# Performance work log

Measured on AMD Instinct MI355X. Metric: run time of the kernel, lower is better.

The kernel has to match this reference:

```python
import jax, jax.numpy as jnp
import numpy as np

T, B, C, N, H = 10, 128, 512, 16, 16
D = C // H          # head dim = 32
HID = 2048          # mlp hidden = 4*dim
TAU, THR, SCALE, ALPHA_MIX = 2.0, 1.0, 0.25, 0.5
SG_ALPHA = 4.0      # surrogate sigmoid alpha

@jax.custom_vjp
def spike_fn(x):
    # heaviside forward, sigmoid surrogate backward (MyGrad / sigmoid.apply)
    return (x > 0).astype(x.dtype)

def _spike_fwd(x):
    return spike_fn(x), x

def _spike_bwd(x, g):
    s = jax.nn.sigmoid(SG_ALPHA * x)
    return (g * SG_ALPHA * s * (1.0 - s),)

spike_fn.defvjp(_spike_fwd, _spike_bwd)

def lif(x):
    # multi-step LIF over leading T axis; mem_detach=True => no BPTT through mem
    def step(mem, inp):
        mem = jax.lax.stop_gradient(mem)
        mem = mem + (inp - mem) / TAU
        s = spike_fn(mem - THR)
        mem = mem * (1.0 - jax.lax.stop_gradient(s))
        return mem, s
    return jax.lax.scan(step, jnp.zeros_like(x[0]), x)[1]

def lif_step(mem, inp):
    # single-step LIF (step=1, layer_by_layer=False); state persists across calls
    mem = jax.lax.stop_gradient(mem)
    mem = mem + (inp - mem) / TAU
    s = spike_fn(mem - THR)
    mem = mem * (1.0 - jax.lax.stop_gradient(s))
    return s, mem

def bn(x, p):
    # eval-mode BatchNorm1d over channel dim; x: (T,B,C,N), p: (4,C)=gamma,beta,mean,var
    g, b, m, v = p
    inv = g * jax.lax.rsqrt(v + 1e-5)
    return (x - m[None, None, :, None]) * inv[None, None, :, None] + b[None, None, :, None]

def conv1x1(x, W):
    # Conv1d k=1 == channel GEMM; x: (T,B,Cin,N), W: (Cout,Cin)
    return jnp.einsum('oc,tbcn->tbon', W, x)

def ssa(x, Wq, bn_q, Wk, bn_k, Wv, bn_v, Wproj, bn_proj, ti_w, ti_b):
    def qkv(W, p):
        y = lif(bn(conv1x1(x, W), p))                       # (T,B,C,N) spikes
        # faithful to torch: raw reshape (T,B,C,N)->(T,B,N,H,D) then permute
        return y.reshape(T, B, N, H, D).transpose(0, 1, 3, 2, 4)  # (T,B,H,N,D)
    q = qkv(Wq, bn_q)
    k = qkv(Wk, bn_k)
    v = qkv(Wv, bn_v)

    out0 = (q[0] @ jnp.swapaxes(k[0], -2, -1) * SCALE) @ v[0]   # (B,H,N,D)

    def step(carry, qkv_t):
        q_ti, mem1, mem2 = carry
        qt, kt, vt = qkv_t
        c = q_ti.reshape(B * H, N, D)
        c = jax.lax.conv_general_dilated(
            c, ti_w, (1,), ((2, 2),), dimension_numbers=('NCH', 'OIH', 'NCH'))
        c = c + ti_b[None, :, None]
        c = c.reshape(B, H, N, D)
        s1, mem1 = lif_step(mem1, c)
        mix = s1 * ALPHA_MIX + qt * (1.0 - ALPHA_MIX)
        s2, mem2 = lif_step(mem2, mix)
        attn = (s2 @ jnp.swapaxes(kt, -2, -1) * SCALE) @ vt
        return (s2, mem1, mem2), attn

    init = (q[0], jnp.zeros_like(q[0]), jnp.zeros_like(q[0]))
    _, outs = jax.lax.scan(step, init, (q[1:], k[1:], v[1:]))
    out = jnp.concatenate([out0[None], outs], axis=0)           # (T,B,H,N,D)

    y = jnp.swapaxes(out, 3, 4).reshape(T, B, C, N)
    y = lif(y)                                                  # attn_lif
    y = lif(bn(conv1x1(y, Wproj), bn_proj))                     # proj
    return y

def mlp(x, W1, b1, bn1, W2, b2, bn2):
    h = lif(bn(conv1x1(x, W1) + b1[None, None, :, None], bn1))
    return lif(bn(conv1x1(h, W2) + b2[None, None, :, None], bn2))

def block(x, Wq, Wk, Wv, Wproj, bn_q, bn_k, bn_v, bn_proj, ti_w, ti_b,
          W1, b1, bn1, W2, b2, bn2):
    x = x + ssa(x, Wq, bn_q, Wk, bn_k, Wv, bn_v, Wproj, bn_proj, ti_w, ti_b)
    x = x + mlp(x, W1, b1, bn1, W2, b2, bn2)
    return x

def setup_inputs() -> dict:
    key = jax.random.key(0)
    ks = jax.random.split(key, 16)

    def w(k, o, i):
        return (jax.random.normal(k, (o, i), jnp.float32) / np.float32(np.sqrt(i)))

    def bnp(k, c):
        k1, k2, k3, k4 = jax.random.split(k, 4)
        return jnp.stack([
            jax.random.uniform(k1, (c,), jnp.float32) + 0.5,   # gamma
            jax.random.normal(k2, (c,), jnp.float32) * 0.1,    # beta
            jax.random.normal(k3, (c,), jnp.float32) * 0.1,    # running mean
            jax.random.uniform(k4, (c,), jnp.float32) + 0.5,   # running var
        ])

    return {
        'x': jax.random.normal(ks[0], (T, B, C, N), jnp.float32),
        'Wq': w(ks[1], C, C), 'Wk': w(ks[2], C, C), 'Wv': w(ks[3], C, C),
        'Wproj': w(ks[4], C, C),
        'bn_q': bnp(ks[5], C), 'bn_k': bnp(ks[6], C), 'bn_v': bnp(ks[7], C),
        'bn_proj': bnp(ks[8], C),
        'ti_w': jax.random.normal(ks[9], (16, 16, 5), jnp.float32) / np.float32(np.sqrt(16 * 5)),
        'ti_b': jax.random.normal(ks[10], (16,), jnp.float32) * 0.1,
        'W1': w(ks[11], HID, C), 'b1': jax.random.normal(ks[12], (HID,), jnp.float32) * 0.1,
        'bn1': bnp(ks[13], HID),
        'W2': w(ks[14], C, HID), 'b2': jax.random.normal(ks[15], (C,), jnp.float32) * 0.1,
        'bn2': bnp(jax.random.fold_in(key, 99), C),
    }

def reference(x, Wq, Wk, Wv, Wproj, bn_q, bn_k, bn_v, bn_proj, ti_w, ti_b,
              W1, b1, bn1, W2, b2, bn2):
    return block(x, Wq, Wk, Wv, Wproj, bn_q, bn_k, bn_v, bn_proj, ti_w, ti_b,
                 W1, b1, bn1, W2, b2, bn2)
```

## Files before the change

kernel.cpp:

```cpp
#include <hip/hip_runtime.h>
#include <cstdint>
#include <cstddef>

#define T_   10
#define B_   128
#define CH_  512
#define N_   16
#define H_   16
#define HID_ 2048
#define TB_  (T_ * B_)

#define BS_PKT   0
#define BS_BF16T 1
#define EP_QKV  0
#define EP_SPK  1
#define EP_HS   2
#define EP_OUT  3

typedef __attribute__((ext_vector_type(8))) short bf16x8;
typedef __attribute__((ext_vector_type(4))) float f32x4;
typedef unsigned short u16;
typedef unsigned long long u64;

__device__ __forceinline__ short f2b(float f) {
    uint32_t u = __float_as_uint(f);
    return (short)((u + 0x7FFFu + ((u >> 16) & 1u)) >> 16);
}
__device__ __forceinline__ float b2f(short s) {
    return __uint_as_float(((uint32_t)(uint16_t)s) << 16);
}

__global__ void fold2(const float* __restrict__ W, const float* __restrict__ bnp,
                      const float* __restrict__ eb, int M, int K, int o0,
                      short* __restrict__ Ah, short* __restrict__ Al,
                      float* __restrict__ bias) {
    int idx = blockIdx.x * 256 + threadIdx.x;
    if (idx >= M * K) return;
    int o = idx / K, k = idx - o * K;
    float g  = bnp[o];
    float be = bnp[M + o];
    float mu = bnp[2 * M + o];
    float va = bnp[3 * M + o];
    float inv = g * (1.0f / sqrtf(va + 1e-5f));
    float w = W[idx] * inv;
    short h = f2b(w);
    Ah[(size_t)(o0 + o) * K + k] = h;
    Al[(size_t)(o0 + o) * K + k] = f2b(w - b2f(h));
    if (k == 0) bias[o0 + o] = ((eb ? eb[o] : 0.0f) - mu) * inv + be;
}

__global__ __launch_bounds__(256) void splitx(
    const float* __restrict__ X, const u16* __restrict__ S,
    short* __restrict__ Bh, short* __restrict__ Bl) {
    __shared__ float xs[8192];
    const int slab = blockIdx.x;
    const int tid  = threadIdx.x;
    const int t    = slab / B_;
    const int b    = slab - t * B_;
    const float* xp = X + (size_t)slab * 8192;
    for (int i = tid; i < 2048; i += 256) {
        float4 v = *(const float4*)&xp[i * 4];
        if (S) {
            union { u16 s[4]; uint2 v; } sw;
            sw.v = *(const uint2*)&S[(size_t)b * 8192 + i * 4];
            v.x += (float)((sw.s[0] >> t) & 1);
            v.y += (float)((sw.s[1] >> t) & 1);
            v.z += (float)((sw.s[2] >> t) & 1);
            v.w += (float)((sw.s[3] >> t) & 1);
        }
        *(float4*)&xs[i * 4] = v;
    }
    __syncthreads();
    const int n = tid & 15, kc = tid >> 4;
    size_t orow = ((size_t)slab * 16 + n) * 512 + kc * 32;
#pragma unroll
    for (int i8 = 0; i8 < 4; ++i8) {
        union { short s[8]; uint4 v; } hb, lb;
#pragma unroll
        for (int j = 0; j < 8; ++j) {
            float v = xs[(kc * 32 + i8 * 8 + j) * 16 + n];
            short h = f2b(v);
            hb.s[j] = h;
            lb.s[j] = f2b(v - b2f(h));
        }
        *(uint4*)&Bh[orow + i8 * 8] = hb.v;
        *(uint4*)&Bl[orow + i8 * 8] = lb.v;
    }
}

template <int R, int GX, int BS, int EPI>
__global__ __launch_bounds__(256, 2) void gemm_mfma(
    const short* __restrict__ Ah, const short* __restrict__ Al,
    const float* __restrict__ bias,
    const short* __restrict__ Bh, const short* __restrict__ Bl,
    const u16* __restrict__ Bu,
    u16* __restrict__ O0, u16* __restrict__ O1, u16* __restrict__ O2,
    float* __restrict__ Oout, const float* __restrict__ Xr,
    const u16* __restrict__ Sr, int K) {
    constexpr int NP = (BS == BS_PKT) ? 2 : 3;
    __shared__ __align__(16) short Bs[(NP == 3 ? 2 : 1) * 6400];
    short* BsH = Bs;
    short* BsL = Bs + 6400;
    const int tid  = threadIdx.x;
    const int lane = tid & 63;
    const int wv   = tid >> 6;
    const int fid  = blockIdx.x;
    const int xcd  = fid & 7;
    const int slot = fid >> 3;
    const int brow = slot / GX;
    const int xb   = slot - brow * GX;
    const int b    = (brow << 3) | xcd;
    const int l15  = lane & 15;
    const int q    = lane >> 4;
    const int row0 = xb * (R * 64) + wv * (R * 16);

    f32x4 acc[R][10];
#pragma unroll
    for (int r = 0; r < R; ++r)
#pragma unroll
        for (int t = 0; t < 10; ++t) acc[r][t] = 0.0f;

    for (int k0 = 0; k0 < K; k0 += 32) {
        __syncthreads();
        if constexpr (BS == BS_PKT) {
            if (tid < 128) {
                int qu = tid & 3, n = (tid >> 2) & 15, half = tid >> 6;
                size_t g = ((size_t)b * 16 + n) * (size_t)K + k0 + qu * 8;
                union { u16 s[8]; uint4 v; } w;
                w.v = *(const uint4*)&Bu[g];
                const int t0 = half * 5;
#pragma unroll
                for (int tt = 0; tt < 5; ++tt) {
                    int t = t0 + tt;
                    union { short s[8]; uint4 v; } hb;
#pragma unroll
                    for (int j = 0; j < 8; ++j)
                        hb.s[j] = ((w.s[j] >> t) & 1) ? (short)0x3F80 : (short)0;
                    *(uint4*)&BsH[(t * 16 + n) * 40 + qu * 8] = hb.v;
                }
            }
        } else {
            for (int idx = tid; idx < 640; idx += 256) {
                int qu = idx & 3, n = (idx >> 2) & 15, t = idx >> 6;
                size_t g = ((size_t)(t * B_ + b) * 16 + n) * (size_t)K + k0 + qu * 8;
                *(uint4*)&BsH[(t * 16 + n) * 40 + qu * 8] = *(const uint4*)&Bh[g];
                *(uint4*)&BsL[(t * 16 + n) * 40 + qu * 8] = *(const uint4*)&Bl[g];
            }
        }
        __syncthreads();
        bf16x8 ah[R], al[R];
#pragma unroll
        for (int r = 0; r < R; ++r) {
            size_t ga = (size_t)(row0 + r * 16 + l15) * K + k0 + q * 8;
            ah[r] = *(const bf16x8*)&Ah[ga];
            al[r] = *(const bf16x8*)&Al[ga];
        }
#pragma unroll
        for (int t = 0; t < 10; ++t) {
            bf16x8 bh = *(const bf16x8*)&BsH[(t * 16 + l15) * 40 + q * 8];
            bf16x8 bl;
            if constexpr (NP == 3) bl = *(const bf16x8*)&BsL[(t * 16 + l15) * 40 + q * 8];
#pragma unroll
            for (int r = 0; r < R; ++r) {
                acc[r][t] = __builtin_amdgcn_mfma_f32_16x16x32_bf16(ah[r], bh, acc[r][t], 0, 0, 0);
                acc[r][t] = __builtin_amdgcn_mfma_f32_16x16x32_bf16(al[r], bh, acc[r][t], 0, 0, 0);
                if constexpr (NP == 3)
                    acc[r][t] = __builtin_amdgcn_mfma_f32_16x16x32_bf16(ah[r], bl, acc[r][t], 0, 0, 0);
            }
        }
    }

    const int tok = l15;
#pragma unroll
    for (int r = 0; r < R; ++r) {
        u16 m4[4];
#pragma unroll
        for (int reg = 0; reg < 4; ++reg) {
            const int row = row0 + r * 16 + q * 4 + reg;
            const float bsv = bias[row];
            u16 sv = 0;
            if constexpr (EPI == EP_OUT) sv = Sr[(size_t)b * 8192 + (size_t)row * 16 + tok];
            float mem = 0.0f;
            u16 msk = 0;
#pragma unroll
            for (int t = 0; t < 10; ++t) {
                float u = acc[r][t][reg] + bsv;
                mem += (u - mem) * 0.5f;
                bool s = mem > 1.0f;
                if (s) mem = 0.0f;
                msk |= (u16)((s ? 1u : 0u) << t);
                if constexpr (EPI == EP_OUT) {
                    size_t off = (size_t)(t * B_ + b) * 8192 + (size_t)row * 16 + tok;
                    Oout[off] = Xr[off] + (float)((sv >> t) & 1) + (s ? 1.0f : 0.0f);
                }
            }
            if constexpr (EPI == EP_QKV) {
                int tsr = row >> 9;
                int c   = row & 511;
                int hh  = (c & 31) >> 1;
                int dd  = ((c & 1) << 4) | tok;
                int nn  = c >> 5;
                u16* qp = (tsr == 0) ? O0 : ((tsr == 1) ? O1 : O2);
                qp[(size_t)b * 8192 + (size_t)hh * 512 + dd * 16 + nn] = msk;
            } else if constexpr (EPI == EP_SPK) {
                O0[(size_t)b * 8192 + (size_t)row * 16 + tok] = msk;
            } else if constexpr (EPI == EP_HS) {
                m4[reg] = msk;
            }
        }
        if constexpr (EPI == EP_HS) {
            union { u16 s[4]; uint2 v; } pk;
            pk.s[0] = m4[0]; pk.s[1] = m4[1]; pk.s[2] = m4[2]; pk.s[3] = m4[3];
            *(uint2*)&O0[((size_t)b * 16 + tok) * 2048 + row0 + r * 16 + q * 4] = pk.v;
        }
    }
}

__global__ __launch_bounds__(256, 1) void scan_kernel(
    const u16* __restrict__ qs, const u16* __restrict__ ks,
    const u16* __restrict__ vs, const float* __restrict__ tiw,
    const float* __restrict__ tib, u16* __restrict__ y1pk) {
    __shared__ float qS[4][36 * 20];
    __shared__ float kS[4][32 * 20];
    __shared__ float vS[4][32 * 20];
    __shared__ float qbS[4][32 * 20];
    __shared__ float A[4][16 * 17];
    const int l  = threadIdx.x & 63;
    const int w  = threadIdx.x >> 6;
    const int b  = blockIdx.y;
    const int h  = blockIdx.x * 4 + w;
    const int n  = l & 15, dg = l >> 4;
    float* qSw  = qS[w];
    float* kSw  = kS[w];
    float* vSw  = vS[w];
    float* qbSw = qbS[w];
    float* Aw   = A[w];

    float wreg[80];
#pragma unroll
    for (int j = 0; j < 80; ++j) wreg[j] = tiw[n * 80 + j];
    const float tibr = tib[n];

    if (l < 40) { qSw[l] = 0.0f; qSw[680 + l] = 0.0f; }

    const size_t base = (size_t)b * 8192 + (size_t)h * 512 + (size_t)l * 8;
    union { u16 s[8]; uint4 v; } qw, kw, vw;
    qw.v = *(const uint4*)&qs[base];
    kw.v = *(const uint4*)&ks[base];
    vw.v = *(const uint4*)&vs[base];

#pragma unroll
    for (int j = 0; j < 8; ++j) {
        int f = l * 8 + j, d = f >> 4, m = f & 15;
        qSw[(d + 2) * 20 + m] = (float)(qw.s[j] & 1);
        kSw[d * 20 + m]       = (float)(kw.s[j] & 1);
        vSw[d * 20 + m]       = (float)(vw.s[j] & 1);
    }

    float mem1[8] = {}, mem2[8] = {}, mem3[8] = {};
    u16 ym[8] = {};

    auto attn_step = [&](int t) {
        float dots[4] = {0.0f, 0.0f, 0.0f, 0.0f};
#pragma unroll
        for (int d = 0; d < 32; ++d) {
            float qv = qSw[(d + 2) * 20 + n];
#pragma unroll
            for (int jj = 0; jj < 4; ++jj)
                dots[jj] = fmaf(qv, kSw[d * 20 + dg * 4 + jj], dots[jj]);
        }
#pragma unroll
        for (int jj = 0; jj < 4; ++jj) Aw[n * 17 + dg * 4 + jj] = dots[jj] * 0.25f;
        float o[8] = {};
#pragma unroll
        for (int m = 0; m < 16; ++m) {
            float av = Aw[n * 17 + m];
#pragma unroll
            for (int dd = 0; dd < 8; ++dd)
                o[dd] = fmaf(av, vSw[(dg * 8 + dd) * 20 + m], o[dd]);
        }
#pragma unroll
        for (int dd = 0; dd < 8; ++dd) {
            mem3[dd] += (o[dd] - mem3[dd]) * 0.5f;
            bool s3 = mem3[dd] > 1.0f;
            if (s3) mem3[dd] = 0.0f;
            ym[dd] |= (u16)((s3 ? 1u : 0u) << t);
        }
    };

    attn_step(0);

    for (int t = 1; t < T_; ++t) {
#pragma unroll
        for (int j = 0; j < 8; ++j) {
            int f = l * 8 + j, d = f >> 4, m = f & 15;
            qbSw[d * 20 + m] = (float)((qw.s[j] >> t) & 1);
            kSw[d * 20 + m]  = (float)((kw.s[j] >> t) & 1);
            vSw[d * 20 + m]  = (float)((vw.s[j] >> t) & 1);
        }
        float c[8];
#pragma unroll
        for (int dd = 0; dd < 8; ++dd) c[dd] = tibr;
#pragma unroll
        for (int x = 0; x < 12; ++x) {
            const float* rp = &qSw[(dg * 8 + x) * 20];
            float qrow[16];
            *(float4*)&qrow[0]  = *(const float4*)&rp[0];
            *(float4*)&qrow[4]  = *(const float4*)&rp[4];
            *(float4*)&qrow[8]  = *(const float4*)&rp[8];
            *(float4*)&qrow[12] = *(const float4*)&rp[12];
#pragma unroll
            for (int k = 0; k < 5; ++k) {
                const int o = x - k;
                if (o >= 0 && o < 8) {
#pragma unroll
                    for (int i = 0; i < 16; ++i)
                        c[o] = fmaf(wreg[i * 5 + k], qrow[i], c[o]);
                }
            }
        }
#pragma unroll
        for (int dd = 0; dd < 8; ++dd) {
            mem1[dd] += (c[dd] - mem1[dd]) * 0.5f;
            bool s1 = mem1[dd] > 1.0f;
            if (s1) mem1[dd] = 0.0f;
            float qb = qbSw[(dg * 8 + dd) * 20 + n];
            float mix = 0.5f * (s1 ? 1.0f : 0.0f) + 0.5f * qb;
            mem2[dd] += (mix - mem2[dd]) * 0.5f;
            bool s2 = mem2[dd] > 1.0f;
            if (s2) mem2[dd] = 0.0f;
            qSw[(dg * 8 + dd + 2) * 20 + n] = s2 ? 1.0f : 0.0f;
        }
        attn_step(t);
    }

    union { u16 s[8]; uint4 v; } yv;
#pragma unroll
    for (int dd = 0; dd < 8; ++dd) yv.s[dd] = ym[dd];
    *(uint4*)&y1pk[((size_t)b * 16 + n) * 512 + h * 32 + dg * 8] = yv.v;
}

extern "C" void kernel_launch(void* const* d_in, const int* in_sizes, int n_in,
                              void* d_out, int out_size, void* d_ws, size_t ws_size,
                              hipStream_t stream) {
    const float* x    = (const float*)d_in[0];
    const float* Wq   = (const float*)d_in[1];
    const float* Wk   = (const float*)d_in[2];
    const float* Wv   = (const float*)d_in[3];
    const float* Wp   = (const float*)d_in[4];
    const float* bnq  = (const float*)d_in[5];
    const float* bnk  = (const float*)d_in[6];
    const float* bnv  = (const float*)d_in[7];
    const float* bnpj = (const float*)d_in[8];
    const float* tiw  = (const float*)d_in[9];
    const float* tib  = (const float*)d_in[10];
    const float* W1   = (const float*)d_in[11];
    const float* b1   = (const float*)d_in[12];
    const float* bn1  = (const float*)d_in[13];
    const float* W2   = (const float*)d_in[14];
    const float* b2   = (const float*)d_in[15];
    const float* bn2  = (const float*)d_in[16];
    float* out = (float*)d_out;

    char* ws = (char*)d_ws;
    size_t cur = 0;
    auto alloc = [&](size_t bytes) -> void* {
        void* p = ws + cur;
        cur = (cur + bytes + 255) & ~(size_t)255;
        return p;
    };
    const size_t PKQ = (size_t)B_ * 8192;
    u16* qpk  = (u16*)alloc(4 * PKQ * 2);
    u16* kpk  = qpk + PKQ;
    u16* vpk  = qpk + 2 * PKQ;
    u16* y1pk = qpk + 3 * PKQ;
    u16* hspk = qpk;
    u16* spk  = (u16*)alloc(PKQ * 2);
    short* BhT = (short*)alloc((size_t)TB_ * 16 * 512 * 2);
    short* BlT = (short*)alloc((size_t)TB_ * 16 * 512 * 2);
    short* Ah_qkv = (short*)alloc((size_t)1536 * 512 * 2);
    short* Al_qkv = (short*)alloc((size_t)1536 * 512 * 2);
    short* Ah_p   = (short*)alloc((size_t)512 * 512 * 2);
    short* Al_p   = (short*)alloc((size_t)512 * 512 * 2);
    short* Ah_1   = (short*)alloc((size_t)2048 * 512 * 2);
    short* Al_1   = (short*)alloc((size_t)2048 * 512 * 2);
    short* Ah_2   = (short*)alloc((size_t)512 * 2048 * 2);
    short* Al_2   = (short*)alloc((size_t)512 * 2048 * 2);
    float* bs_qkv = (float*)alloc(1536 * 4);
    float* bs_p   = (float*)alloc(512 * 4);
    float* bs_1   = (float*)alloc(2048 * 4);
    float* bs_2   = (float*)alloc(512 * 4);

    fold2<<<1024, 256, 0, stream>>>(Wq, bnq, nullptr, 512, 512, 0,    Ah_qkv, Al_qkv, bs_qkv);
    fold2<<<1024, 256, 0, stream>>>(Wk, bnk, nullptr, 512, 512, 512,  Ah_qkv, Al_qkv, bs_qkv);
    fold2<<<1024, 256, 0, stream>>>(Wv, bnv, nullptr, 512, 512, 1024, Ah_qkv, Al_qkv, bs_qkv);
    fold2<<<1024, 256, 0, stream>>>(Wp, bnpj, nullptr, 512, 512, 0,   Ah_p, Al_p, bs_p);
    fold2<<<4096, 256, 0, stream>>>(W1, bn1, b1, 2048, 512, 0,        Ah_1, Al_1, bs_1);
    fold2<<<4096, 256, 0, stream>>>(W2, bn2, b2, 512, 2048, 0,        Ah_2, Al_2, bs_2);

    splitx<<<TB_, 256, 0, stream>>>(x, nullptr, BhT, BlT);
    gemm_mfma<4, 6, BS_BF16T, EP_QKV><<<6 * B_, 256, 0, stream>>>(
        Ah_qkv, Al_qkv, bs_qkv, BhT, BlT, nullptr, qpk, kpk, vpk,
        nullptr, nullptr, nullptr, 512);
    scan_kernel<<<dim3(4, B_), 256, 0, stream>>>(qpk, kpk, vpk, tiw, tib, y1pk);
    gemm_mfma<2, 4, BS_PKT, EP_SPK><<<4 * B_, 256, 0, stream>>>(
        Ah_p, Al_p, bs_p, nullptr, nullptr, y1pk, spk, nullptr, nullptr,
        nullptr, nullptr, nullptr, 512);

    splitx<<<TB_, 256, 0, stream>>>(x, spk, BhT, BlT);
    gemm_mfma<4, 8, BS_BF16T, EP_HS><<<8 * B_, 256, 0, stream>>>(
        Ah_1, Al_1, bs_1, BhT, BlT, nullptr, hspk, nullptr, nullptr,
        nullptr, nullptr, nullptr, 512);
    gemm_mfma<2, 4, BS_PKT, EP_OUT><<<4 * B_, 256, 0, stream>>>(
        Ah_2, Al_2, bs_2, nullptr, nullptr, hspk, nullptr, nullptr, nullptr,
        out, x, spk, 2048);
}
```

Measured before the change: 625.3 us.

## Split GEMM into specialized bf16 and packed-spike kernels with restructured B staging

Splits the templated MFMA GEMM into two kernels. The bf16 path now loops over timesteps outermost and stages a full K=512 slab per timestep in LDS, which cuts per-k barriers. Its A fragments are reloaded from global memory for every timestep, so A traffic rises tenfold. The packed-spike path loads the whole packed B row set into LDS once, with no barriers in the K loop, and expands bits to bf16 in registers using a multiply trick. This removes the per-k shared writes and syncs.

```diff
diff --git a/kernel.cpp b/kernel.cpp
--- a/kernel.cpp
+++ b/kernel.cpp
@@ -10,8 +10,6 @@
 #define HID_ 2048
 #define TB_  (T_ * B_)
 
-#define BS_PKT   0
-#define BS_BF16T 1
 #define EP_QKV  0
 #define EP_SPK  1
 #define EP_HS   2
@@ -88,19 +86,16 @@
     }
 }
 
-template <int R, int GX, int BS, int EPI>
-__global__ __launch_bounds__(256, 2) void gemm_mfma(
+template <int R, int GX, int EPI>
+__global__ __launch_bounds__(256, 2) void gemm_bf16t(
     const short* __restrict__ Ah, const short* __restrict__ Al,
     const float* __restrict__ bias,
     const short* __restrict__ Bh, const short* __restrict__ Bl,
-    const u16* __restrict__ Bu,
-    u16* __restrict__ O0, u16* __restrict__ O1, u16* __restrict__ O2,
-    float* __restrict__ Oout, const float* __restrict__ Xr,
-    const u16* __restrict__ Sr, int K) {
-    constexpr int NP = (BS == BS_PKT) ? 2 : 3;
-    __shared__ __align__(16) short Bs[(NP == 3 ? 2 : 1) * 6400];
-    short* BsH = Bs;
-    short* BsL = Bs + 6400;
+    u16* __restrict__ O0, u16* __restrict__ O1, u16* __restrict__ O2) {
+    constexpr int KT  = 512;
+    constexpr int SLB = 648;
+    __shared__ __align__(16) short BsH[16 * SLB];
+    __shared__ __align__(16) short BsL[16 * SLB];
     const int tid  = threadIdx.x;
     const int lane = tid & 63;
     const int wv   = tid >> 6;
@@ -120,52 +115,130 @@
 #pragma unroll
         for (int t = 0; t < 10; ++t) acc[r][t] = 0.0f;
 
-    for (int k0 = 0; k0 < K; k0 += 32) {
+#pragma unroll
+    for (int p = 0; p < 10; ++p) {
         __syncthreads();
-        if constexpr (BS == BS_PKT) {
-            if (tid < 128) {
-                int qu = tid & 3, n = (tid >> 2) & 15, half = tid >> 6;
-                size_t g = ((size_t)b * 16 + n) * (size_t)K + k0 + qu * 8;
-                union { u16 s[8]; uint4 v; } w;
-                w.v = *(const uint4*)&Bu[g];
-                const int t0 = half * 5;
-#pragma unroll
-                for (int tt = 0; tt < 5; ++tt) {
-                    int t = t0 + tt;
-                    union { short s[8]; uint4 v; } hb;
-#pragma unroll
-                    for (int j = 0; j < 8; ++j)
-                        hb.s[j] = ((w.s[j] >> t) & 1) ? (short)0x3F80 : (short)0;
-                    *(uint4*)&BsH[(t * 16 + n) * 40 + qu * 8] = hb.v;
-                }
-            }
-        } else {
-            for (int idx = tid; idx < 640; idx += 256) {
-                int qu = idx & 3, n = (idx >> 2) & 15, t = idx >> 6;
-                size_t g = ((size_t)(t * B_ + b) * 16 + n) * (size_t)K + k0 + qu * 8;
-                *(uint4*)&BsH[(t * 16 + n) * 40 + qu * 8] = *(const uint4*)&Bh[g];
-                *(uint4*)&BsL[(t * 16 + n) * 40 + qu * 8] = *(const uint4*)&Bl[g];
-            }
+        for (int idx = tid; idx < 1024; idx += 256) {
+            int c8 = idx & 63, n = idx >> 6;
+            size_t g = ((size_t)(p * B_ + b) * 16 + n) * KT + c8 * 8;
+            int lo = (c8 >> 2) * SLB + n * 40 + (c8 & 3) * 8;
+            *(uint4*)&BsH[lo] = *(const uint4*)&Bh[g];
+            *(uint4*)&BsL[lo] = *(const uint4*)&Bl[g];
         }
         __syncthreads();
+#pragma unroll
+        for (int kk = 0; kk < 16; ++kk) {
+            const int k0 = kk * 32;
+            bf16x8 ah[R], al[R];
+#pragma unroll
+            for (int r = 0; r < R; ++r) {
+                size_t ga = (size_t)(row0 + r * 16 + l15) * KT + k0 + q * 8;
+                ah[r] = *(const bf16x8*)&Ah[ga];
+                al[r] = *(const bf16x8*)&Al[ga];
+            }
+            bf16x8 bh = *(const bf16x8*)&BsH[kk * SLB + l15 * 40 + q * 8];
+            bf16x8 bl = *(const bf16x8*)&BsL[kk * SLB + l15 * 40 + q * 8];
+#pragma unroll
+            for (int r = 0; r < R; ++r) {
+                acc[r][p] = __builtin_amdgcn_mfma_f32_16x16x32_bf16(ah[r], bh, acc[r][p], 0, 0, 0);
+                acc[r][p] = __builtin_amdgcn_mfma_f32_16x16x32_bf16(al[r], bh, acc[r][p], 0, 0, 0);
+                acc[r][p] = __builtin_amdgcn_mfma_f32_16x16x32_bf16(ah[r], bl, acc[r][p], 0, 0, 0);
+            }
+        }
+    }
+
+    const int tok = l15;
+#pragma unroll
+    for (int r = 0; r < R; ++r) {
+        u16 m4[4];
+#pragma unroll
+        for (int reg = 0; reg < 4; ++reg) {
+            const int row = row0 + r * 16 + q * 4 + reg;
+            const float bsv = bias[row];
+            float mem = 0.0f;
+            u16 msk = 0;
+#pragma unroll
+            for (int t = 0; t < 10; ++t) {
+                float u = acc[r][t][reg] + bsv;
+                mem += (u - mem) * 0.5f;
+                bool s = mem > 1.0f;
+                if (s) mem = 0.0f;
+                msk |= (u16)((s ? 1u : 0u) << t);
+            }
+            if constexpr (EPI == EP_QKV) {
+                int tsr = row >> 9;
+                int c   = row & 511;
+                int hh  = (c & 31) >> 1;
+                int dd  = ((c & 1) << 4) | tok;
+                int nn  = c >> 5;
+                u16* qp = (tsr == 0) ? O0 : ((tsr == 1) ? O1 : O2);
+                qp[(size_t)b * 8192 + (size_t)hh * 512 + dd * 16 + nn] = msk;
+            } else {
+                m4[reg] = msk;
+            }
+        }
+        if constexpr (EPI == EP_HS) {
+            union { u16 s[4]; uint2 v; } pk;
+            pk.s[0] = m4[0]; pk.s[1] = m4[1]; pk.s[2] = m4[2]; pk.s[3] = m4[3];
+            *(uint2*)&O0[((size_t)b * 16 + tok) * 2048 + row0 + r * 16 + q * 4] = pk.v;
+        }
+    }
+}
+
+template <int R, int GX, int EPI, int KT>
+__global__ __launch_bounds__(256, 2) void gemm_pkt(
+    const short* __restrict__ Ah, const short* __restrict__ Al,
+    const float* __restrict__ bias, const u16* __restrict__ Bu,
+    u16* __restrict__ O0, float* __restrict__ Oout,
+    const float* __restrict__ Xr, const u16* __restrict__ Sr) {
+    constexpr int K8 = KT / 8;
+    __shared__ __align__(16) u16 Bp[K8 * 136];
+    const int tid  = threadIdx.x;
+    const int lane = tid & 63;
+    const int wv   = tid >> 6;
+    const int fid  = blockIdx.x;
+    const int xcd  = fid & 7;
+    const int slot = fid >> 3;
+    const int brow = slot / GX;
+    const int xb   = slot - brow * GX;
+    const int b    = (brow << 3) | xcd;
+    const int l15  = lane & 15;
+    const int q    = lane >> 4;
+    const int row0 = xb * (R * 64) + wv * (R * 16);
+
+    for (int idx = tid; idx < 16 * K8; idx += 256) {
+        int kc = idx & (K8 - 1), n = idx / K8;
+        *(uint4*)&Bp[kc * 136 + n * 8] =
+            *(const uint4*)&Bu[((size_t)b * 16 + n) * KT + kc * 8];
+    }
+    __syncthreads();
+
+    f32x4 acc[R][10];
+#pragma unroll
+    for (int r = 0; r < R; ++r)
+#pragma unroll
+        for (int t = 0; t < 10; ++t) acc[r][t] = 0.0f;
+
+    for (int k0 = 0; k0 < KT; k0 += 32) {
         bf16x8 ah[R], al[R];
 #pragma unroll
         for (int r = 0; r < R; ++r) {
-            size_t ga = (size_t)(row0 + r * 16 + l15) * K + k0 + q * 8;
+            size_t ga = (size_t)(row0 + r * 16 + l15) * KT + k0 + q * 8;
             ah[r] = *(const bf16x8*)&Ah[ga];
             al[r] = *(const bf16x8*)&Al[ga];
         }
+        union { uint32_t u[4]; uint4 v; } w;
+        w.v = *(const uint4*)&Bp[(k0 / 8 + q) * 136 + l15 * 8];
 #pragma unroll
         for (int t = 0; t < 10; ++t) {
-            bf16x8 bh = *(const bf16x8*)&BsH[(t * 16 + l15) * 40 + q * 8];
-            bf16x8 bl;
-            if constexpr (NP == 3) bl = *(const bf16x8*)&BsL[(t * 16 + l15) * 40 + q * 8];
+            union { uint32_t u[4]; bf16x8 h; } bh;
+#pragma unroll
+            for (int j = 0; j < 4; ++j)
+                bh.u[j] = ((w.u[j] >> t) & 0x00010001u) * 0x3F80u;
 #pragma unroll
             for (int r = 0; r < R; ++r) {
-                acc[r][t] = __builtin_amdgcn_mfma_f32_16x16x32_bf16(ah[r], bh, acc[r][t], 0, 0, 0);
-                acc[r][t] = __builtin_amdgcn_mfma_f32_16x16x32_bf16(al[r], bh, acc[r][t], 0, 0, 0);
-                if constexpr (NP == 3)
-                    acc[r][t] = __builtin_amdgcn_mfma_f32_16x16x32_bf16(ah[r], bl, acc[r][t], 0, 0, 0);
+                acc[r][t] = __builtin_amdgcn_mfma_f32_16x16x32_bf16(ah[r], bh.h, acc[r][t], 0, 0, 0);
+                acc[r][t] = __builtin_amdgcn_mfma_f32_16x16x32_bf16(al[r], bh.h, acc[r][t], 0, 0, 0);
             }
         }
     }
@@ -173,7 +246,6 @@
     const int tok = l15;
 #pragma unroll
     for (int r = 0; r < R; ++r) {
-        u16 m4[4];
 #pragma unroll
         for (int reg = 0; reg < 4; ++reg) {
             const int row = row0 + r * 16 + q * 4 + reg;
@@ -194,24 +266,9 @@
                     Oout[off] = Xr[off] + (float)((sv >> t) & 1) + (s ? 1.0f : 0.0f);
                 }
             }
-            if constexpr (EPI == EP_QKV) {
-                int tsr = row >> 9;
-                int c   = row & 511;
-                int hh  = (c & 31) >> 1;
-                int dd  = ((c & 1) << 4) | tok;
-                int nn  = c >> 5;
-                u16* qp = (tsr == 0) ? O0 : ((tsr == 1) ? O1 : O2);
-                qp[(size_t)b * 8192 + (size_t)hh * 512 + dd * 16 + nn] = msk;
-            } else if constexpr (EPI == EP_SPK) {
+            if constexpr (EPI == EP_SPK) {
                 O0[(size_t)b * 8192 + (size_t)row * 16 + tok] = msk;
-            } else if constexpr (EPI == EP_HS) {
-                m4[reg] = msk;
-            }
-        }
-        if constexpr (EPI == EP_HS) {
-            union { u16 s[4]; uint2 v; } pk;
-            pk.s[0] = m4[0]; pk.s[1] = m4[1]; pk.s[2] = m4[2]; pk.s[3] = m4[3];
-            *(uint2*)&O0[((size_t)b * 16 + tok) * 2048 + row0 + r * 16 + q * 4] = pk.v;
+            }
         }
     }
 }
@@ -399,19 +456,15 @@
     fold2<<<4096, 256, 0, stream>>>(W2, bn2, b2, 512, 2048, 0,        Ah_2, Al_2, bs_2);
 
     splitx<<<TB_, 256, 0, stream>>>(x, nullptr, BhT, BlT);
-    gemm_mfma<4, 6, BS_BF16T, EP_QKV><<<6 * B_, 256, 0, stream>>>(
-        Ah_qkv, Al_qkv, bs_qkv, BhT, BlT, nullptr, qpk, kpk, vpk,
-        nullptr, nullptr, nullptr, 512);
+    gemm_bf16t<4, 6, EP_QKV><<<6 * B_, 256, 0, stream>>>(
+        Ah_qkv, Al_qkv, bs_qkv, BhT, BlT, qpk, kpk, vpk);
     scan_kernel<<<dim3(4, B_), 256, 0, stream>>>(qpk, kpk, vpk, tiw, tib, y1pk);
-    gemm_mfma<2, 4, BS_PKT, EP_SPK><<<4 * B_, 256, 0, stream>>>(
-        Ah_p, Al_p, bs_p, nullptr, nullptr, y1pk, spk, nullptr, nullptr,
-        nullptr, nullptr, nullptr, 512);
+    gemm_pkt<2, 4, EP_SPK, 512><<<4 * B_, 256, 0, stream>>>(
+        Ah_p, Al_p, bs_p, y1pk, spk, nullptr, nullptr, nullptr);
 
     splitx<<<TB_, 256, 0, stream>>>(x, spk, BhT, BlT);
-    gemm_mfma<4, 8, BS_BF16T, EP_HS><<<8 * B_, 256, 0, stream>>>(
-        Ah_1, Al_1, bs_1, BhT, BlT, nullptr, hspk, nullptr, nullptr,
-        nullptr, nullptr, nullptr, 512);
-    gemm_mfma<2, 4, BS_PKT, EP_OUT><<<4 * B_, 256, 0, stream>>>(
-        Ah_2, Al_2, bs_2, nullptr, nullptr, hspk, nullptr, nullptr, nullptr,
-        out, x, spk, 2048);
-}
+    gemm_bf16t<4, 8, EP_HS><<<8 * B_, 256, 0, stream>>>(
+        Ah_1, Al_1, bs_1, BhT, BlT, hspk, nullptr, nullptr);
+    gemm_pkt<2, 4, EP_OUT, 2048><<<4 * B_, 256, 0, stream>>>(
+        Ah_2, Al_2, bs_2, hspk, nullptr, out, x, spk);
+}
```

Result: slower. 1.372 ms (+119.4%).
